# Kernel optimization log

Measured on AMD Instinct MI355X. Metric: run time of the kernel, lower is better.

The kernel has to match this reference:

```python
import jax, jax.numpy as jnp
import numpy as np

D, H, W = 16, 16, 16          # token grid = img_size/patch_size at i_layer=0
NUM_HEADS = 8
DISTANCE = 10.0               # 10 - i_layer


def _local_pattern(d, h, w, distance):
    # faithful to local_nd_pattern: meshgrid (ij), flatten, cdist p=2, < distance
    g = jnp.meshgrid(jnp.arange(d), jnp.arange(h), jnp.arange(w), indexing='ij')
    coords = jnp.stack([c.reshape(-1) for c in g], axis=1).astype(jnp.float32)  # [N,3]
    diff = coords[:, None, :] - coords[None, :, :]                               # [N,N,3]
    dist = jnp.sqrt(jnp.sum(diff * diff, axis=-1))
    return dist < distance                                                       # [N,N] bool


def setup_inputs() -> dict:
    key = jax.random.key(0)
    k1, k2, k3 = jax.random.split(key, 3)
    dim = 256
    x = jax.random.normal(k1, (1, dim, D, H, W), dtype=jnp.float32)
    qkv_w = jax.random.normal(k2, (3 * dim, dim), dtype=jnp.float32) * (dim ** -0.5)
    proj_w = jax.random.normal(k3, (dim, dim), dtype=jnp.float32) * (dim ** -0.5)
    proj_b = jnp.zeros((dim,), dtype=jnp.float32)
    return {"x": x, "qkv_w": qkv_w, "proj_w": proj_w, "proj_b": proj_b}


def reference(x, qkv_w, proj_w, proj_b):
    b, c, d, h, w = x.shape
    n = d * h * w
    hd = c // NUM_HEADS
    mask = _local_pattern(d, h, w, DISTANCE)                  # [N,N] bool

    # b c d h w -> b (dhw) c
    tok = x.reshape(b, c, n).transpose(0, 2, 1)               # [B,N,C]
    qkv = jnp.einsum('bnc,oc->bno', tok, qkv_w)               # [B,N,3C]
    qkv = qkv.reshape(b, n, 3, NUM_HEADS, hd)
    qkv = qkv.transpose(2, 0, 3, 1, 4)                        # [3,B,H,N,hd]
    q, k, v = qkv[0], qkv[1], qkv[2]                          # [B,H,N,hd]

    scale = 1.0 / jnp.sqrt(jnp.asarray(hd, dtype=x.dtype))
    scores = jnp.einsum('bhnd,bhmd->bhnm', q, k) * scale      # [B,H,N,N]
    scores = jnp.where(mask[None, None], scores, -jnp.inf)
    attn = jax.nn.softmax(scores, axis=-1)
    out = jnp.einsum('bhnm,bhmd->bhnd', attn, v)              # [B,H,N,hd]

    out = out.transpose(0, 2, 1, 3).reshape(b, n, c)          # [B,N,C]
    out = jnp.einsum('bnc,oc->bno', out, proj_w) + proj_b
    # b (dhw) c -> b c d h w
    out = out.transpose(0, 2, 1).reshape(b, c, d, h, w)
    return out
```

## Files before the change

### kernel.cpp

```cpp
#include <hip/hip_runtime.h>
#include <hip/hip_bf16.h>

typedef __attribute__((ext_vector_type(8))) short short8;
typedef __attribute__((ext_vector_type(4))) float floatx4;

#define L2E 1.4426950408889634f

#if __has_builtin(__builtin_amdgcn_exp2f)
#define EXP2(x) __builtin_amdgcn_exp2f(x)
#else
#define EXP2(x) exp2f(x)
#endif
#if __has_builtin(__builtin_amdgcn_rcpf)
#define RCP(x) __builtin_amdgcn_rcpf(x)
#else
#define RCP(x) (1.0f / (x))
#endif

static __device__ __forceinline__ unsigned short f2bf(float f) {
    unsigned int u = __builtin_bit_cast(unsigned int, f);
    u += 0x7fffu + ((u >> 16) & 1u);
    return (unsigned short)(u >> 16);
}
static __device__ __forceinline__ unsigned int pk_bf16(float a, float b) {
    __hip_bfloat162 h2 = __float22bfloat162_rn(make_float2(a, b));
    unsigned int u;
    __builtin_memcpy(&u, &h2, 4);
    return u;
}

__global__ __launch_bounds__(256) void k_qkv(const float* __restrict__ x,
                                             const float* __restrict__ qw,
                                             unsigned short* __restrict__ qm,
                                             unsigned short* __restrict__ km,
                                             unsigned short* __restrict__ vt) {
    __shared__ __align__(16) unsigned short At[64][136];
    __shared__ __align__(16) unsigned short Wt[64][136];
    const int tid = threadIdx.x;
    const int wave = tid >> 6, lane = tid & 63;
    const int l16 = lane & 15, quad = lane >> 4;
    const int m0 = blockIdx.x * 64;
    const int o0 = blockIdx.y * 64;

    floatx4 acc[4] = {};
    for (int rnd = 0; rnd < 2; ++rnd) {
        const int cbase = rnd * 128;
        if (rnd) __syncthreads();
        {
            const int tok0 = (tid & 15) * 4;
            const int c0   = (tid >> 4) * 8;
            const float* xp = x + (size_t)(cbase + c0) * 4096 + m0 + tok0;
            float4 v[8];
            #pragma unroll
            for (int j = 0; j < 8; ++j)
                v[j] = *reinterpret_cast<const float4*>(xp + (size_t)j * 4096);
            #pragma unroll
            for (int t = 0; t < 4; ++t) {
                unsigned int d[4];
                d[0] = pk_bf16((&v[0].x)[t], (&v[1].x)[t]);
                d[1] = pk_bf16((&v[2].x)[t], (&v[3].x)[t]);
                d[2] = pk_bf16((&v[4].x)[t], (&v[5].x)[t]);
                d[3] = pk_bf16((&v[6].x)[t], (&v[7].x)[t]);
                __builtin_memcpy(&At[tok0 + t][c0], d, 16);
            }
        }
        {
            const int o_l = tid >> 2, cp = (tid & 3) * 32;
            const float4* wp = reinterpret_cast<const float4*>(
                qw + (size_t)(o0 + o_l) * 256 + cbase + cp);
            #pragma unroll
            for (int j = 0; j < 2; ++j) {
                const float4 g0 = wp[4 * j + 0], g1 = wp[4 * j + 1];
                const float4 g2 = wp[4 * j + 2], g3 = wp[4 * j + 3];
                unsigned int u[8];
                u[0] = pk_bf16(g0.x, g0.y); u[1] = pk_bf16(g0.z, g0.w);
                u[2] = pk_bf16(g1.x, g1.y); u[3] = pk_bf16(g1.z, g1.w);
                u[4] = pk_bf16(g2.x, g2.y); u[5] = pk_bf16(g2.z, g2.w);
                u[6] = pk_bf16(g3.x, g3.y); u[7] = pk_bf16(g3.z, g3.w);
                __builtin_memcpy(&Wt[o_l][cp + 16 * j], u, 32);
            }
        }
        __syncthreads();
        #pragma unroll
        for (int cc = 0; cc < 4; ++cc) {
            const int c0 = cc * 32 + quad * 8;
            const short8 a = *reinterpret_cast<const short8*>(&At[wave * 16 + l16][c0]);
            #pragma unroll
            for (int t4 = 0; t4 < 4; ++t4) {
                const short8 b = *reinterpret_cast<const short8*>(&Wt[t4 * 16 + l16][c0]);
                acc[t4] = __builtin_amdgcn_mfma_f32_16x16x32_bf16(a, b, acc[t4], 0, 0, 0);
            }
        }
    }

    const int s = o0 >> 8;
    if (s < 2) {
        const float qscale = 0.17677669529663687f * L2E;
        #pragma unroll
        for (int t4 = 0; t4 < 4; ++t4) {
            #pragma unroll
            for (int r = 0; r < 4; ++r) {
                const int n = m0 + wave * 16 + quad * 4 + r;
                const int o = o0 + t4 * 16 + l16;
                const int rem = o & 255, head = rem >> 5, t = rem & 31;
                if (s == 0)  qm[((size_t)head * 4096 + n) * 32 + t] = f2bf(acc[t4][r] * qscale);
                else         km[((size_t)head * 4096 + n) * 32 + t] = f2bf(acc[t4][r]);
            }
        }
    } else {
        __syncthreads();
        unsigned short (*Ct)[72] = reinterpret_cast<unsigned short(*)[72]>(&At[0][0]);
        #pragma unroll
        for (int t4 = 0; t4 < 4; ++t4) {
            unsigned int d2[2];
            d2[0] = pk_bf16(acc[t4][0], acc[t4][1]);
            d2[1] = pk_bf16(acc[t4][2], acc[t4][3]);
            __builtin_memcpy(&Ct[t4 * 16 + l16][wave * 16 + quad * 4], d2, 8);
        }
        __syncthreads();
        const int row = tid >> 2, col0 = (tid & 3) * 16;
        unsigned short* dst = vt + (size_t)(o0 - 512 + row) * 4096 + m0 + col0;
        const short8 ca = *reinterpret_cast<const short8*>(&Ct[row][col0]);
        const short8 cb = *reinterpret_cast<const short8*>(&Ct[row][col0 + 8]);
        *reinterpret_cast<short8*>(dst) = ca;
        *reinterpret_cast<short8*>(dst + 8) = cb;
    }
}

__global__ __launch_bounds__(256, 2) void k_attn(const unsigned short* __restrict__ qm,
                                                 const unsigned short* __restrict__ km,
                                                 const unsigned short* __restrict__ vt,
                                                 unsigned short* __restrict__ ao) {
    const int h   = blockIdx.y;
    const int nq0 = blockIdx.x * 64;
    const int tid = threadIdx.x;
    const int wv  = tid >> 6;
    const int lane = tid & 63;
    const int l16 = lane & 15, quad = lane >> 4;
    const int nqw = nq0 + wv * 16;

    __shared__ __align__(16) unsigned short Kt[2][2048];
    __shared__ __align__(16) unsigned short Vt[2][2048];
    __shared__ __align__(16) unsigned short PT[4][16][72];

    const short8 a_q = *reinterpret_cast<const short8*>(
        qm + ((size_t)h * 4096 + nqw + l16) * 32 + quad * 8);

    const int hq = (nqw >> 4) & 15;
    const int dq = nq0 >> 8;
    float dw2[4];
    #pragma unroll
    for (int r = 0; r < 4; ++r) {
        const float dw = (float)(quad * 4 + r - l16);
        dw2[r] = dw * dw;
    }

    const int dk_lo = (dq > 9) ? dq - 9 : 0;
    const int dk_hi = (dq < 6) ? dq + 9 : 15;
    const int NT = 4 * (dk_hi - dk_lo + 1);

    const int skey = tid >> 2;
    const int sdo  = (tid & 3) * 8;
    const int sdim = tid >> 3;
    const int skg  = tid & 7;
    const unsigned short* ksrc = km + ((size_t)h << 17) + skey * 32 + sdo;
    const unsigned short* vsrc = vt + (((size_t)h * 32 + sdim) << 12) + skg * 8;
    const int kdst = (skey * 32 + sdo) ^ ((skey & 7) << 3);
    const int vdst = (skg * 256 + sdim * 8) ^ (skg << 3);

    float l_acc = 0.f;
    floatx4 o_acc[2] = {};

#define J0T(T) (((dk_lo + ((T) >> 2)) << 8) + (((T) & 3) << 6))

    short8 gK, gV;
    {
        const int j0 = J0T(0);
        gK = *reinterpret_cast<const short8*>(ksrc + (size_t)j0 * 32);
        gV = *reinterpret_cast<const short8*>(vsrc + j0);
        *reinterpret_cast<short8*>(&Kt[0][kdst]) = gK;
        *reinterpret_cast<short8*>(&Vt[0][vdst]) = gV;
        const int j1 = J0T(1);
        gK = *reinterpret_cast<const short8*>(ksrc + (size_t)j1 * 32);
        gV = *reinterpret_cast<const short8*>(vsrc + j1);
    }
    __syncthreads();

    for (int t = 0; t < NT; ++t) {
        const int cb = t & 1, nb = cb ^ 1;

        *reinterpret_cast<short8*>(&Kt[nb][kdst]) = gK;
        *reinterpret_cast<short8*>(&Vt[nb][vdst]) = gV;

        {
            const int tn = (t + 2 < NT) ? t + 2 : NT - 1;
            const int j2 = J0T(tn);
            gK = *reinterpret_cast<const short8*>(ksrc + (size_t)j2 * 32);
            gV = *reinterpret_cast<const short8*>(vsrc + j2);
        }

        {
            const int dk = dk_lo + (t >> 2), g = t & 3;
            const int dd = dq - dk;
            const int bb = 100 - dd * dd;
            const int h0 = hq - 4 * g;
            int thr[4];
            thr[0] = bb - h0 * h0;
            thr[1] = bb - (h0 - 1) * (h0 - 1);
            thr[2] = bb - (h0 - 2) * (h0 - 2);
            thr[3] = bb - (h0 - 3) * (h0 - 3);

            if (thr[0] > 0 || thr[1] > 0 || thr[2] > 0 || thr[3] > 0) {
                #pragma unroll
                for (int t4 = 0; t4 < 4; ++t4) {
                    const bool sib = (thr[t4 ^ 1] > 0);
                    if (thr[t4] > 0) {
                        const short8 kf = *reinterpret_cast<const short8*>(
                            &Kt[cb][((t4 * 16 + l16) * 32 + quad * 8) ^ ((l16 & 7) << 3)]);
                        const floatx4 sf = __builtin_amdgcn_mfma_f32_16x16x32_bf16(
                            kf, a_q, (floatx4){0.f, 0.f, 0.f, 0.f}, 0, 0, 0);
                        const float thrf = (float)thr[t4];
                        const float p0 = (dw2[0] < thrf) ? EXP2(sf[0]) : 0.f;
                        const float p1 = (dw2[1] < thrf) ? EXP2(sf[1]) : 0.f;
                        const float p2 = (dw2[2] < thrf) ? EXP2(sf[2]) : 0.f;
                        const float p3 = (dw2[3] < thrf) ? EXP2(sf[3]) : 0.f;
                        l_acc += (p0 + p1) + (p2 + p3);
                        unsigned int pair[2];
                        pair[0] = pk_bf16(p0, p1);
                        pair[1] = pk_bf16(p2, p3);
                        __builtin_memcpy(&PT[wv][l16][t4 * 16 + quad * 4], pair, 8);
                    } else if (sib) {
                        const unsigned int zz[2] = {0u, 0u};
                        __builtin_memcpy(&PT[wv][l16][t4 * 16 + quad * 4], zz, 8);
                    }
                }
                #pragma unroll
                for (int kt = 0; kt < 2; ++kt) {
                    if (thr[2 * kt] > 0 || thr[2 * kt + 1] > 0) {
                        const short8 b_p = *reinterpret_cast<const short8*>(
                            &PT[wv][l16][kt * 32 + quad * 8]);
                        const int kg = kt * 4 + quad;
                        #pragma unroll
                        for (int hf = 0; hf < 2; ++hf) {
                            const short8 vf = *reinterpret_cast<const short8*>(
                                &Vt[cb][(kg * 256 + (hf * 16 + l16) * 8) ^ (kg << 3)]);
                            o_acc[hf] = __builtin_amdgcn_mfma_f32_16x16x32_bf16(
                                vf, b_p, o_acc[hf], 0, 0, 0);
                        }
                    }
                }
            }
        }
        __syncthreads();
    }
#undef J0T

    l_acc += __shfl_xor(l_acc, 16);
    l_acc += __shfl_xor(l_acc, 32);
    const float inv = RCP(l_acc);
    #pragma unroll
    for (int hf = 0; hf < 2; ++hf) {
        unsigned int uu[2];
        uu[0] = pk_bf16(o_acc[hf][0] * inv, o_acc[hf][1] * inv);
        uu[1] = pk_bf16(o_acc[hf][2] * inv, o_acc[hf][3] * inv);
        __builtin_memcpy(ao + (size_t)(nqw + l16) * 256 + h * 32 + hf * 16 + quad * 4,
                         uu, 8);
    }
}

__global__ __launch_bounds__(256) void k_proj(const unsigned short* __restrict__ ao,
                                              const float* __restrict__ pw,
                                              const float* __restrict__ pb,
                                              float* __restrict__ out) {
    __shared__ __align__(16) unsigned short Pt[64][264];
    const int tid = threadIdx.x;
    const int wave = tid >> 6, lane = tid & 63;
    const int l16 = lane & 15, quad = lane >> 4;
    const int n0 = blockIdx.x * 32;
    const int m0 = blockIdx.y * 64;

    {
        const int o_l = tid >> 2, cp = (tid & 3) * 64;
        const float4* wp = reinterpret_cast<const float4*>(pw + (size_t)(m0 + o_l) * 256 + cp);
        #pragma unroll
        for (int j = 0; j < 4; ++j) {
            const float4 g0 = wp[4 * j + 0], g1 = wp[4 * j + 1];
            const float4 g2 = wp[4 * j + 2], g3 = wp[4 * j + 3];
            unsigned int u[8];
            u[0] = pk_bf16(g0.x, g0.y); u[1] = pk_bf16(g0.z, g0.w);
            u[2] = pk_bf16(g1.x, g1.y); u[3] = pk_bf16(g1.z, g1.w);
            u[4] = pk_bf16(g2.x, g2.y); u[5] = pk_bf16(g2.z, g2.w);
            u[6] = pk_bf16(g3.x, g3.y); u[7] = pk_bf16(g3.z, g3.w);
            __builtin_memcpy(&Pt[o_l][cp + 16 * j], u, 32);
        }
    }
    __syncthreads();

    floatx4 acc[2] = {};
    #pragma unroll
    for (int cc = 0; cc < 8; ++cc) {
        const int c0 = cc * 32 + quad * 8;
        const short8 a = *reinterpret_cast<const short8*>(&Pt[wave * 16 + l16][c0]);
        #pragma unroll
        for (int t4 = 0; t4 < 2; ++t4) {
            const short8 b = *reinterpret_cast<const short8*>(
                ao + (size_t)(n0 + t4 * 16 + l16) * 256 + c0);
            acc[t4] = __builtin_amdgcn_mfma_f32_16x16x32_bf16(a, b, acc[t4], 0, 0, 0);
        }
    }
    #pragma unroll
    for (int t4 = 0; t4 < 2; ++t4) {
        #pragma unroll
        for (int r = 0; r < 4; ++r) {
            const int o = m0 + wave * 16 + quad * 4 + r;
            const int n = n0 + t4 * 16 + l16;
            out[(size_t)o * 4096 + n] = acc[t4][r] + pb[o];
        }
    }
}

extern "C" void kernel_launch(void* const* d_in, const int* in_sizes, int n_in,
                              void* d_out, int out_size, void* d_ws, size_t ws_size,
                              hipStream_t stream) {
    const float* x      = (const float*)d_in[0];
    const float* qkv_w  = (const float*)d_in[1];
    const float* proj_w = (const float*)d_in[2];
    const float* proj_b = (const float*)d_in[3];
    float* out = (float*)d_out;

    char* B = (char*)d_ws;
    const size_t MB = 1u << 20;
    unsigned short* ao = (unsigned short*)(B);
    unsigned short* qm = (unsigned short*)(B + 2 * MB);
    unsigned short* km = (unsigned short*)(B + 4 * MB);
    unsigned short* vt = (unsigned short*)(B + 6 * MB);

    k_qkv<<<dim3(64, 12), 256, 0, stream>>>(x, qkv_w, qm, km, vt);
    k_attn<<<dim3(64, 8), 256, 0, stream>>>(qm, km, vt, ao);
    k_proj<<<dim3(128, 4), 256, 0, stream>>>(ao, proj_w, proj_b, out);
}
```

Baseline: 150.7 us.

## Process two key tiles per barrier with branchless masking and split accumulators

The attention loop now stages two 64-key tiles per iteration into doubled shared buffers, so each barrier covers two tiles and global prefetch runs two tiles ahead. The per-tile mask skip branches are removed, so every tile is computed unconditionally with elementwise masking. Separate output accumulators per slot break the MFMA dependency chain and are summed at the end. This trades extra LDS (roughly double), extra registers and wasted MFMA/exp work on fully masked tiles for fewer barriers and more instruction-level parallelism.

After: 136.4 us. 1.1x faster.

```diff
diff --git a/kernel.cpp b/kernel.cpp
--- a/kernel.cpp
+++ b/kernel.cpp
@@ -139,9 +139,9 @@
     const int l16 = lane & 15, quad = lane >> 4;
     const int nqw = nq0 + wv * 16;
 
-    __shared__ __align__(16) unsigned short Kt[2][2048];
-    __shared__ __align__(16) unsigned short Vt[2][2048];
-    __shared__ __align__(16) unsigned short PT[4][16][72];
+    __shared__ __align__(16) unsigned short Kt[2][2][2048];
+    __shared__ __align__(16) unsigned short Vt[2][2][2048];
+    __shared__ __align__(16) unsigned short PT[4][2][16][72];
 
     const short8 a_q = *reinterpret_cast<const short8*>(
         qm + ((size_t)h * 4096 + nqw + l16) * 32 + quad * 8);
@@ -169,90 +169,93 @@
     const int vdst = (skg * 256 + sdim * 8) ^ (skg << 3);
 
     float l_acc = 0.f;
-    floatx4 o_acc[2] = {};
+    floatx4 o_acc[2][2] = {};
 
 #define J0T(T) (((dk_lo + ((T) >> 2)) << 8) + (((T) & 3) << 6))
 
-    short8 gK, gV;
-    {
-        const int j0 = J0T(0);
-        gK = *reinterpret_cast<const short8*>(ksrc + (size_t)j0 * 32);
-        gV = *reinterpret_cast<const short8*>(vsrc + j0);
-        *reinterpret_cast<short8*>(&Kt[0][kdst]) = gK;
-        *reinterpret_cast<short8*>(&Vt[0][vdst]) = gV;
-        const int j1 = J0T(1);
-        gK = *reinterpret_cast<const short8*>(ksrc + (size_t)j1 * 32);
-        gV = *reinterpret_cast<const short8*>(vsrc + j1);
-    }
+    short8 rK[2], rV[2];
+#define LOAD2(TA, TB) {                                                   \
+        const int ja_ = J0T(TA), jb_ = J0T(TB);                           \
+        rK[0] = *reinterpret_cast<const short8*>(ksrc + (size_t)ja_ * 32);\
+        rV[0] = *reinterpret_cast<const short8*>(vsrc + ja_);             \
+        rK[1] = *reinterpret_cast<const short8*>(ksrc + (size_t)jb_ * 32);\
+        rV[1] = *reinterpret_cast<const short8*>(vsrc + jb_);             \
+    }
+#define WRITE2(NB) {                                                      \
+        *reinterpret_cast<short8*>(&Kt[NB][0][kdst]) = rK[0];             \
+        *reinterpret_cast<short8*>(&Vt[NB][0][vdst]) = rV[0];             \
+        *reinterpret_cast<short8*>(&Kt[NB][1][kdst]) = rK[1];             \
+        *reinterpret_cast<short8*>(&Vt[NB][1][vdst]) = rV[1];             \
+    }
+
+#define SSTAGE(T, CB, SL) {                                               \
+        const int dk_ = dk_lo + ((T) >> 2), g_ = (T) & 3;                 \
+        const int dd_ = dq - dk_;                                         \
+        const int bb_ = 100 - dd_ * dd_;                                  \
+        const int h0_ = hq - 4 * g_;                                      \
+        int th_[4];                                                       \
+        th_[0] = bb_ - h0_ * h0_;                                         \
+        th_[1] = bb_ - (h0_ - 1) * (h0_ - 1);                             \
+        th_[2] = bb_ - (h0_ - 2) * (h0_ - 2);                             \
+        th_[3] = bb_ - (h0_ - 3) * (h0_ - 3);                             \
+        _Pragma("unroll")                                                 \
+        for (int t4 = 0; t4 < 4; ++t4) {                                  \
+            const short8 kf = *reinterpret_cast<const short8*>(           \
+                &Kt[CB][SL][((t4 * 16 + l16) * 32 + quad * 8) ^ ((l16 & 7) << 3)]); \
+            const floatx4 sf = __builtin_amdgcn_mfma_f32_16x16x32_bf16(   \
+                kf, a_q, (floatx4){0.f, 0.f, 0.f, 0.f}, 0, 0, 0);         \
+            const float thrf = (float)th_[t4];                            \
+            const float p0 = (dw2[0] < thrf) ? EXP2(sf[0]) : 0.f;         \
+            const float p1 = (dw2[1] < thrf) ? EXP2(sf[1]) : 0.f;         \
+            const float p2 = (dw2[2] < thrf) ? EXP2(sf[2]) : 0.f;         \
+            const float p3 = (dw2[3] < thrf) ? EXP2(sf[3]) : 0.f;         \
+            l_acc += (p0 + p1) + (p2 + p3);                               \
+            unsigned int pair_[2];                                        \
+            pair_[0] = pk_bf16(p0, p1);                                   \
+            pair_[1] = pk_bf16(p2, p3);                                   \
+            __builtin_memcpy(&PT[wv][SL][l16][t4 * 16 + quad * 4], pair_, 8); \
+        }                                                                 \
+    }
+
+#define PVST(CB, SL) {                                                    \
+        _Pragma("unroll")                                                 \
+        for (int kt = 0; kt < 2; ++kt) {                                  \
+            const short8 b_p = *reinterpret_cast<const short8*>(          \
+                &PT[wv][SL][l16][kt * 32 + quad * 8]);                    \
+            const int kg = kt * 4 + quad;                                 \
+            _Pragma("unroll")                                             \
+            for (int hf = 0; hf < 2; ++hf) {                              \
+                const short8 vf = *reinterpret_cast<const short8*>(       \
+                    &Vt[CB][SL][(kg * 256 + (hf * 16 + l16) * 8) ^ (kg << 3)]); \
+                o_acc[SL][hf] = __builtin_amdgcn_mfma_f32_16x16x32_bf16(  \
+                    vf, b_p, o_acc[SL][hf], 0, 0, 0);                     \
+            }                                                             \
+        }                                                                 \
+    }
+
+    LOAD2(0, 1)
+    WRITE2(0)
+    LOAD2(2, 3)
     __syncthreads();
 
-    for (int t = 0; t < NT; ++t) {
-        const int cb = t & 1, nb = cb ^ 1;
-
-        *reinterpret_cast<short8*>(&Kt[nb][kdst]) = gK;
-        *reinterpret_cast<short8*>(&Vt[nb][vdst]) = gV;
-
+    for (int t2 = 0; t2 < NT; t2 += 2) {
+        const int cb = (t2 >> 1) & 1, nb = cb ^ 1;
+        WRITE2(nb)
         {
-            const int tn = (t + 2 < NT) ? t + 2 : NT - 1;
-            const int j2 = J0T(tn);
-            gK = *reinterpret_cast<const short8*>(ksrc + (size_t)j2 * 32);
-            gV = *reinterpret_cast<const short8*>(vsrc + j2);
-        }
-
-        {
-            const int dk = dk_lo + (t >> 2), g = t & 3;
-            const int dd = dq - dk;
-            const int bb = 100 - dd * dd;
-            const int h0 = hq - 4 * g;
-            int thr[4];
-            thr[0] = bb - h0 * h0;
-            thr[1] = bb - (h0 - 1) * (h0 - 1);
-            thr[2] = bb - (h0 - 2) * (h0 - 2);
-            thr[3] = bb - (h0 - 3) * (h0 - 3);
-
-            if (thr[0] > 0 || thr[1] > 0 || thr[2] > 0 || thr[3] > 0) {
-                #pragma unroll
-                for (int t4 = 0; t4 < 4; ++t4) {
-                    const bool sib = (thr[t4 ^ 1] > 0);
-                    if (thr[t4] > 0) {
-                        const short8 kf = *reinterpret_cast<const short8*>(
-                            &Kt[cb][((t4 * 16 + l16) * 32 + quad * 8) ^ ((l16 & 7) << 3)]);
-                        const floatx4 sf = __builtin_amdgcn_mfma_f32_16x16x32_bf16(
-                            kf, a_q, (floatx4){0.f, 0.f, 0.f, 0.f}, 0, 0, 0);
-                        const float thrf = (float)thr[t4];
-                        const float p0 = (dw2[0] < thrf) ? EXP2(sf[0]) : 0.f;
-                        const float p1 = (dw2[1] < thrf) ? EXP2(sf[1]) : 0.f;
-                        const float p2 = (dw2[2] < thrf) ? EXP2(sf[2]) : 0.f;
-                        const float p3 = (dw2[3] < thrf) ? EXP2(sf[3]) : 0.f;
-                        l_acc += (p0 + p1) + (p2 + p3);
-                        unsigned int pair[2];
-                        pair[0] = pk_bf16(p0, p1);
-                        pair[1] = pk_bf16(p2, p3);
-                        __builtin_memcpy(&PT[wv][l16][t4 * 16 + quad * 4], pair, 8);
-                    } else if (sib) {
-                        const unsigned int zz[2] = {0u, 0u};
-                        __builtin_memcpy(&PT[wv][l16][t4 * 16 + quad * 4], zz, 8);
-                    }
-                }
-                #pragma unroll
-                for (int kt = 0; kt < 2; ++kt) {
-                    if (thr[2 * kt] > 0 || thr[2 * kt + 1] > 0) {
-                        const short8 b_p = *reinterpret_cast<const short8*>(
-                            &PT[wv][l16][kt * 32 + quad * 8]);
-                        const int kg = kt * 4 + quad;
-                        #pragma unroll
-                        for (int hf = 0; hf < 2; ++hf) {
-                            const short8 vf = *reinterpret_cast<const short8*>(
-                                &Vt[cb][(kg * 256 + (hf * 16 + l16) * 8) ^ (kg << 3)]);
-                            o_acc[hf] = __builtin_amdgcn_mfma_f32_16x16x32_bf16(
-                                vf, b_p, o_acc[hf], 0, 0, 0);
-                        }
-                    }
-                }
-            }
-        }
+            int ta = t2 + 4; if (ta >= NT) ta = NT - 1;
+            int tb = t2 + 5; if (tb >= NT) tb = NT - 1;
+            LOAD2(ta, tb)
+        }
+        SSTAGE(t2,     cb, 0)
+        SSTAGE(t2 + 1, cb, 1)
+        PVST(cb, 0)
+        PVST(cb, 1)
         __syncthreads();
     }
+#undef PVST
+#undef SSTAGE
+#undef WRITE2
+#undef LOAD2
 #undef J0T
 
     l_acc += __shfl_xor(l_acc, 16);
@@ -260,9 +263,10 @@
     const float inv = RCP(l_acc);
     #pragma unroll
     for (int hf = 0; hf < 2; ++hf) {
+        const floatx4 os = o_acc[0][hf] + o_acc[1][hf];
         unsigned int uu[2];
-        uu[0] = pk_bf16(o_acc[hf][0] * inv, o_acc[hf][1] * inv);
-        uu[1] = pk_bf16(o_acc[hf][2] * inv, o_acc[hf][3] * inv);
+        uu[0] = pk_bf16(os[0] * inv, os[1] * inv);
+        uu[1] = pk_bf16(os[2] * inv, os[3] * inv);
         __builtin_memcpy(ao + (size_t)(nqw + l16) * 256 + h * 32 + hf * 16 + quad * 4,
                          uu, 8);
     }
```
